# Kernel tuning notes

Hardware: AMD Instinct MI355X
Metric: run time of the kernel (lower is better)

Reference implementation:

```python
import jax, jax.numpy as jnp
import numpy as np
from jax import lax

H = 128

def _lstm_gates(x, h, c, w_ih, w_hh, b_ih, b_hh):
    # PyTorch gate order: i, f, g, o
    g = x @ w_ih.T + h @ w_hh.T + b_ih + b_hh
    i, f, gg, o = jnp.split(g, 4, axis=-1)
    c_new = jax.nn.sigmoid(f) * c + jax.nn.sigmoid(i) * jnp.tanh(gg)
    h_new = jax.nn.sigmoid(o) * jnp.tanh(c_new)
    return h_new, c_new

def _lstm_layer(x_btF, w_ih, w_hh, b_ih, b_hh):
    B = x_btF.shape[0]
    h0 = jnp.zeros((B, H), x_btF.dtype)
    c0 = jnp.zeros((B, H), x_btF.dtype)
    def step(carry, xt):
        h, c = carry
        h, c = _lstm_gates(xt, h, c, w_ih, w_hh, b_ih, b_hh)
        return (h, c), h
    (h_T, c_T), ys = lax.scan(step, (h0, c0), jnp.swapaxes(x_btF, 0, 1))
    return jnp.swapaxes(ys, 0, 1), h_T, c_T

def setup_inputs() -> dict:
    key = jax.random.key(0)
    ks = jax.random.split(key, 20)
    B, T, D, P = 4096, 200, 2, 3
    s = 1.0 / np.sqrt(H)
    u = lambda k, shp: jax.random.uniform(k, shp, jnp.float32, -s, s)
    return {
        'x_hist': jax.random.normal(ks[0], (B, T, D), jnp.float32),
        'params': jax.random.normal(ks[1], (B, P), jnp.float32),
        'pred_len': 200,
        'w_ih0': u(ks[2], (4 * H, D)), 'w_hh0': u(ks[3], (4 * H, H)),
        'b_ih0': u(ks[4], (4 * H,)), 'b_hh0': u(ks[5], (4 * H,)),
        'w_ih1': u(ks[6], (4 * H, H)), 'w_hh1': u(ks[7], (4 * H, H)),
        'b_ih1': u(ks[8], (4 * H,)), 'b_hh1': u(ks[9], (4 * H,)),
        'dec_w_ih': u(ks[10], (4 * H, D + P)), 'dec_w_hh': u(ks[11], (4 * H, H)),
        'dec_b_ih': u(ks[12], (4 * H,)), 'dec_b_hh': u(ks[13], (4 * H,)),
        'proj_w': u(ks[14], (H, P)), 'proj_b': u(ks[15], (H,)),
        'out_w': u(ks[16], (2, H)), 'out_b': u(ks[17], (2,)),
    }

def reference(x_hist, params, pred_len, w_ih0, w_hh0, b_ih0, b_hh0,
              w_ih1, w_hh1, b_ih1, b_hh1, dec_w_ih, dec_w_hh, dec_b_ih,
              dec_b_hh, proj_w, proj_b, out_w, out_b):
    # 2-layer encoder LSTM; only last layer's final (h, c) are used
    y1, _, _ = _lstm_layer(x_hist, w_ih0, w_hh0, b_ih0, b_hh0)
    _, h_n, c_n = _lstm_layer(y1, w_ih1, w_hh1, b_ih1, b_hh1)
    h = h_n + params @ proj_w.T + proj_b
    c = c_n
    cur = x_hist[:, -1, :]
    def step(carry, _):
        h, c, cur = carry
        inp = jnp.concatenate([cur, params], axis=-1)
        h, c = _lstm_gates(inp, h, c, dec_w_ih, dec_w_hh, dec_b_ih, dec_b_hh)
        cur = h @ out_w.T + out_b
        return (h, c, cur), cur
    _, preds = lax.scan(step, (h, c, cur), None, length=pred_len)
    return jnp.swapaxes(preds, 0, 1)  # [B, pred_len, 2]
```

## Files before the change

kernel.cpp:

```cpp
#include <hip/hip_runtime.h>
#include <stdint.h>

typedef __bf16 bf16x8 __attribute__((ext_vector_type(8)));
typedef float  f32x4  __attribute__((ext_vector_type(4)));

#define PRED   200
#define TSTEPS 200
#define NBLK   256

#define ASTR   280
#define ALO    136
#define ABUFE  (16*ASTR*2)
#define W_BYTES 131072
#define A_OFF   W_BYTES
#define LDS_A   (A_OFF + 2*ABUFE)
#define STG_OFF (A_OFF + 2*ABUFE)
#define LDS_C   (STG_OFF + ABUFE)

#define ABUFD  8192
#define LDS_D  (2*ABUFD)

#define STATE_FLOATS ((size_t)NBLK*4*2048)

__device__ __forceinline__ float sigm(float x){ return 1.0f/(1.0f+__expf(-x)); }
__device__ __forceinline__ float tanhx(float x){
  float t=__expf(-2.0f*fabsf(x)); float y=(1.0f-t)/(1.0f+t); return copysignf(y,x);
}
__device__ __forceinline__ bf16x8 hi8(float4 a, float4 b){
  bf16x8 r; r[0]=(__bf16)a.x; r[1]=(__bf16)a.y; r[2]=(__bf16)a.z; r[3]=(__bf16)a.w;
  r[4]=(__bf16)b.x; r[5]=(__bf16)b.y; r[6]=(__bf16)b.z; r[7]=(__bf16)b.w; return r;
}
__device__ __forceinline__ bf16x8 lo8(float4 a, float4 b, bf16x8 h){
  bf16x8 r;
  r[0]=(__bf16)(a.x-(float)h[0]); r[1]=(__bf16)(a.y-(float)h[1]);
  r[2]=(__bf16)(a.z-(float)h[2]); r[3]=(__bf16)(a.w-(float)h[3]);
  r[4]=(__bf16)(b.x-(float)h[4]); r[5]=(__bf16)(b.y-(float)h[5]);
  r[6]=(__bf16)(b.z-(float)h[6]); r[7]=(__bf16)(b.w-(float)h[7]); return r;
}
#define MFMA(A,B,C) __builtin_amdgcn_mfma_f32_16x16x32_bf16((A),(B),(C),0,0,0)

#define PIN(x) do{ \
  unsigned _w0=((unsigned*)&(x))[0], _w1=((unsigned*)&(x))[1], \
           _w2=((unsigned*)&(x))[2], _w3=((unsigned*)&(x))[3]; \
  asm volatile("" : "+v"(_w0), "+v"(_w1), "+v"(_w2), "+v"(_w3)); \
  ((unsigned*)&(x))[0]=_w0; ((unsigned*)&(x))[1]=_w1; \
  ((unsigned*)&(x))[2]=_w2; ((unsigned*)&(x))[3]=_w3; }while(0)
#define PINF(x) asm volatile("" : "+v"(x))

__device__ __forceinline__ void bar_lds(){
  asm volatile("s_waitcnt lgkmcnt(0)" ::: "memory");
  __builtin_amdgcn_s_barrier();
  asm volatile("" ::: "memory");
}

__device__ __forceinline__ int aoff(int row, int col){
  return row*512 + ((((col>>3) ^ (row&7)) << 4) | ((col&7)<<1));
}
__device__ __forceinline__ int frdoff(int c, int qd, int kt, int plane){
  return c*512 + (((((kt<<2)+qd) ^ (c&7)) | (plane<<4)) << 4);
}

__global__ void __launch_bounds__(512,2)
k_l0(const float* __restrict__ xh, const float* __restrict__ wih0,
     const float* __restrict__ whh0, const float* __restrict__ bih0,
     const float* __restrict__ bhh0, float* __restrict__ wsf,
     int chunkStart, int chunkLen, unsigned long long stageFloats)
{
  extern __shared__ char smem[];
  const int tid=threadIdx.x, wv=tid>>6, l=tid&63, c=l&15, qd=l>>4;
  const int hc=wv*16+c, blk=blockIdx.x, r0=blk*16;
  float* stf = wsf + stageFloats;
  #pragma unroll
  for (int i=0;i<16;++i){
    int f=i*8+wv, ntg=f>>2, kt=f&3;
    int g=(ntg&3)*128+(ntg>>2)*16+c, k=kt*32+qd*8;
    const float* s=whh0+g*128+k;
    *(bf16x8*)(smem+f*1024+l*16)=hi8(*(const float4*)s,*(const float4*)(s+4));
  }
  bf16x8 wlo[16];
  #pragma unroll
  for (int tt=0;tt<4;++tt)
    #pragma unroll
    for (int kt=0;kt<4;++kt){
      const float* s=whh0+(size_t)(tt*128+hc)*128+kt*32+qd*8;
      float4 a=*(const float4*)s, b=*(const float4*)(s+4);
      wlo[tt*4+kt]=lo8(a,b,hi8(a,b));
    }
  #pragma unroll
  for (int i=0;i<16;++i) PIN(wlo[i]);
  float b0[4], w0x[4], w0y[4];
  #pragma unroll
  for (int tt=0;tt<4;++tt){
    int g=tt*128+hc;
    b0[tt]=bih0[g]+bhh0[g]; w0x[tt]=wih0[2*g]; w0y[tt]=wih0[2*g+1];
  }
  float c0[4];
  {
    __bf16* B1=(__bf16*)(smem+A_OFF+ABUFE);
    const float* hst=stf+(size_t)(blk*4+0)*2048;
    const float* cst=stf+(size_t)(blk*4+1)*2048;
    #pragma unroll
    for (int i=0;i<4;++i){
      int e=tid*4+i, row=e>>7, col=e&127;
      float v=0.f; if(chunkStart) v=hst[e];
      __bf16 h=(__bf16)v;
      B1[row*ASTR+col]=h; B1[row*ASTR+ALO+col]=(__bf16)(v-(float)h);
    }
    #pragma unroll
    for (int j=0;j<4;++j){ float v=0.f; if(chunkStart) v=cst[(qd*4+j)*128+hc]; c0[j]=v; }
  }
  __syncthreads();
  float hprev[4];
  float2 xv[4];
  #pragma unroll
  for (int j=0;j<4;++j) xv[j]=*(const float2*)(xh+(size_t)(r0+qd*4+j)*400+chunkStart*2);
  for (int t=0;t<chunkLen;++t){
    const int p=t&1, tg=chunkStart+t;
    if (t){
      float* h0p=wsf+((size_t)(t-1)*NBLK+blk)*2048;
      #pragma unroll
      for (int j=0;j<4;++j) h0p[(qd*4+j)*128+hc]=hprev[j];
    }
    float2 xn[4];
    #pragma unroll
    for (int j=0;j<4;++j) xn[j]=(float2){0.f,0.f};
    if (t+1<chunkLen){
      #pragma unroll
      for (int j=0;j<4;++j) xn[j]=*(const float2*)(xh+(size_t)(r0+qd*4+j)*400+(tg+1)*2);
    }
    f32x4 acc[4];
    #pragma unroll
    for (int tt=0;tt<4;++tt) acc[tt]=(f32x4){b0[tt],b0[tt],b0[tt],b0[tt]};
    const char* Ar=smem+A_OFF+(size_t)(1-p)*ABUFE;
    #pragma unroll
    for (int kt=0;kt<4;++kt){
      bf16x8 ah=*(const bf16x8*)(Ar+(c*ASTR+kt*32+qd*8)*2);
      bf16x8 al=*(const bf16x8*)(Ar+(c*ASTR+ALO+kt*32+qd*8)*2);
      #pragma unroll
      for (int tt=0;tt<4;++tt){
        bf16x8 bh=*(const bf16x8*)(smem+(size_t)((wv*4+tt)*4+kt)*1024+l*16);
        acc[tt]=MFMA(ah,bh,acc[tt]);
        acc[tt]=MFMA(al,bh,acc[tt]);
        acc[tt]=MFMA(ah,wlo[tt*4+kt],acc[tt]);
      }
    }
    __bf16* Aw=(__bf16*)(smem+A_OFF+(size_t)p*ABUFE);
    #pragma unroll
    for (int j=0;j<4;++j){
      float gi=acc[0][j]+xv[j].x*w0x[0]+xv[j].y*w0y[0];
      float gf=acc[1][j]+xv[j].x*w0x[1]+xv[j].y*w0y[1];
      float gg=acc[2][j]+xv[j].x*w0x[2]+xv[j].y*w0y[2];
      float go=acc[3][j]+xv[j].x*w0x[3]+xv[j].y*w0y[3];
      float cn=sigm(gf)*c0[j]+sigm(gi)*tanhx(gg); c0[j]=cn;
      float hn=sigm(go)*tanhx(cn);
      int row=qd*4+j;
      __bf16 hh=(__bf16)hn;
      Aw[row*ASTR+hc]=hh; Aw[row*ASTR+ALO+hc]=(__bf16)(hn-(float)hh);
      hprev[j]=hn;
    }
    #pragma unroll
    for (int j=0;j<4;++j) xv[j]=xn[j];
    bar_lds();
  }
  {
    float* h0p=wsf+((size_t)(chunkLen-1)*NBLK+blk)*2048;
    #pragma unroll
    for (int j=0;j<4;++j){
      int row=qd*4+j;
      h0p[row*128+hc]=hprev[j];
      stf[(size_t)(blk*4+0)*2048+row*128+hc]=hprev[j];
      stf[(size_t)(blk*4+1)*2048+row*128+hc]=c0[j];
    }
  }
}

__global__ void __launch_bounds__(512,2)
k_l1(const float* __restrict__ wih1, const float* __restrict__ whh1,
     const float* __restrict__ bih1, const float* __restrict__ bhh1,
     float* __restrict__ wsf, int chunkStart, int chunkLen,
     unsigned long long stageFloats)
{
  extern __shared__ char smem[];
  const int tid=threadIdx.x, wv=tid>>6, l=tid&63, c=l&15, qd=l>>4;
  const int hc=wv*16+c, blk=blockIdx.x;
  float* stf = wsf + stageFloats;
  #pragma unroll
  for (int i=0;i<16;++i){
    int f=i*8+wv, ntg=f>>2, kt=f&3;
    int g=(ntg&3)*128+(ntg>>2)*16+c, k=kt*32+qd*8;
    const float* s=wih1+g*128+k;
    *(bf16x8*)(smem+f*1024+l*16)=hi8(*(const float4*)s,*(const float4*)(s+4));
  }
  bf16x8 whh[16], whl[16], wil[16];
  #pragma unroll
  for (int tt=0;tt<4;++tt)
    #pragma unroll
    for (int kt=0;kt<4;++kt){
      const float* s2=whh1+(size_t)(tt*128+hc)*128+kt*32+qd*8;
      float4 a2=*(const float4*)s2, b2=*(const float4*)(s2+4);
      bf16x8 h2=hi8(a2,b2);
      whh[tt*4+kt]=h2; whl[tt*4+kt]=lo8(a2,b2,h2);
      const float* s3=wih1+(size_t)(tt*128+hc)*128+kt*32+qd*8;
      float4 a3=*(const float4*)s3, b3=*(const float4*)(s3+4);
      wil[tt*4+kt]=lo8(a3,b3,hi8(a3,b3));
    }
  #pragma unroll
  for (int i=0;i<16;++i){ PIN(whh[i]); PIN(whl[i]); PIN(wil[i]); }
  float b1v[4];
  #pragma unroll
  for (int tt=0;tt<4;++tt){ int g=tt*128+hc; b1v[tt]=bih1[g]+bhh1[g]; }
  float c1[4];
  {
    __bf16* B1=(__bf16*)(smem+A_OFF+ABUFE);
    const float* hst=stf+(size_t)(blk*4+2)*2048;
    const float* cst=stf+(size_t)(blk*4+3)*2048;
    #pragma unroll
    for (int i=0;i<4;++i){
      int e=tid*4+i, row=e>>7, col=e&127;
      float v=0.f; if(chunkStart) v=hst[e];
      __bf16 h=(__bf16)v;
      B1[row*ASTR+col]=h; B1[row*ASTR+ALO+col]=(__bf16)(v-(float)h);
    }
    #pragma unroll
    for (int j=0;j<4;++j){ float v=0.f; if(chunkStart) v=cst[(qd*4+j)*128+hc]; c1[j]=v; }
  }
  float4 r4=*(const float4*)(wsf+((size_t)0*NBLK+blk)*2048+tid*4);
  __syncthreads();
  for (int t=0;t<chunkLen;++t){
    const int p=t&1;
    {
      __bf16* ST=(__bf16*)(smem+STG_OFF);
      int e=tid*4, row=e>>7, col=e&127;
      #pragma unroll
      for (int i=0;i<4;++i){
        float v=((const float*)&r4)[i]; __bf16 h=(__bf16)v;
        ST[row*ASTR+col+i]=h; ST[row*ASTR+ALO+col+i]=(__bf16)(v-(float)h);
      }
    }
    if (t+1<chunkLen) r4=*(const float4*)(wsf+((size_t)(t+1)*NBLK+blk)*2048+tid*4);
    bar_lds();
    f32x4 acc[4];
    #pragma unroll
    for (int tt=0;tt<4;++tt) acc[tt]=(f32x4){b1v[tt],b1v[tt],b1v[tt],b1v[tt]};
    const char* Ar=smem+A_OFF+(size_t)(1-p)*ABUFE;
    const char* Sr=smem+STG_OFF;
    #pragma unroll
    for (int kt=0;kt<4;++kt){
      bf16x8 a0h=*(const bf16x8*)(Sr+(c*ASTR+kt*32+qd*8)*2);
      bf16x8 a0l=*(const bf16x8*)(Sr+(c*ASTR+ALO+kt*32+qd*8)*2);
      bf16x8 a1h=*(const bf16x8*)(Ar+(c*ASTR+kt*32+qd*8)*2);
      bf16x8 a1l=*(const bf16x8*)(Ar+(c*ASTR+ALO+kt*32+qd*8)*2);
      #pragma unroll
      for (int tt=0;tt<4;++tt){
        bf16x8 bh=*(const bf16x8*)(smem+(size_t)((wv*4+tt)*4+kt)*1024+l*16);
        acc[tt]=MFMA(a0h,bh,acc[tt]);
        acc[tt]=MFMA(a0l,bh,acc[tt]);
        acc[tt]=MFMA(a0h,wil[tt*4+kt],acc[tt]);
        acc[tt]=MFMA(a1h,whh[tt*4+kt],acc[tt]);
        acc[tt]=MFMA(a1l,whh[tt*4+kt],acc[tt]);
        acc[tt]=MFMA(a1h,whl[tt*4+kt],acc[tt]);
      }
    }
    __bf16* Aw=(__bf16*)(smem+A_OFF+(size_t)p*ABUFE);
    #pragma unroll
    for (int j=0;j<4;++j){
      float cn=sigm(acc[1][j])*c1[j]+sigm(acc[0][j])*tanhx(acc[2][j]); c1[j]=cn;
      float hn=sigm(acc[3][j])*tanhx(cn);
      int row=qd*4+j;
      __bf16 hh=(__bf16)hn;
      Aw[row*ASTR+hc]=hh; Aw[row*ASTR+ALO+hc]=(__bf16)(hn-(float)hh);
      if (t==chunkLen-1){
        stf[(size_t)(blk*4+2)*2048+row*128+hc]=hn;
        stf[(size_t)(blk*4+3)*2048+row*128+hc]=cn;
      }
    }
    bar_lds();
  }
}

__global__ void __launch_bounds__(512,1)
k_dec(const float* __restrict__ xh, const float* __restrict__ pprm,
      const float* __restrict__ dwihp, const float* __restrict__ dwhh,
      const float* __restrict__ dbih, const float* __restrict__ dbhh,
      const float* __restrict__ pw, const float* __restrict__ pb,
      const float* __restrict__ ow, const float* __restrict__ ob,
      const float* __restrict__ wsf, float* __restrict__ out,
      unsigned long long stageFloats)
{
  extern __shared__ char smem[];
  const int tid=threadIdx.x, wv=tid>>6, l=tid&63, c=l&15, qd=l>>4;
  const int hc=wv*16+c, blk=blockIdx.x, r0=blk*16;
  const float* stf = wsf + stageFloats;
  float ob0=ob[0], ob1=ob[1];
  float prm[4][3];
  #pragma unroll
  for (int j=0;j<4;++j){
    size_t r=(size_t)(r0+qd*4+j);
    prm[j][0]=pprm[r*3+0]; prm[j][1]=pprm[r*3+1]; prm[j][2]=pprm[r*3+2];
  }
  float ptF[4][4], dw0[4], dw1[4];
  #pragma unroll
  for (int tt=0;tt<4;++tt){
    int g=tt*128+hc;
    float db=dbih[g]+dbhh[g];
    dw0[tt]=dwihp[g*5+0]; dw1[tt]=dwihp[g*5+1];
    #pragma unroll
    for (int j=0;j<4;++j)
      ptF[tt][j]=db+prm[j][0]*dwihp[g*5+2]+prm[j][1]*dwihp[g*5+3]+prm[j][2]*dwihp[g*5+4]
                 +dw0[tt]*ob0+dw1[tt]*ob1;
  }
  #pragma unroll
  for (int tt=0;tt<4;++tt)
    #pragma unroll
    for (int j=0;j<4;++j) PINF(ptF[tt][j]);
  bf16x8 whi[16], wlo[16];
  #pragma unroll
  for (int tt=0;tt<4;++tt)
    #pragma unroll
    for (int kt=0;kt<4;++kt){
      int g=tt*128+hc, k=kt*32+qd*8;
      float4 a=*(const float4*)(dwhh+(size_t)g*128+k), b=*(const float4*)(dwhh+(size_t)g*128+k+4);
      float4 o0a=*(const float4*)(ow+k),     o0b=*(const float4*)(ow+k+4);
      float4 o1a=*(const float4*)(ow+128+k), o1b=*(const float4*)(ow+128+k+4);
      a.x+=dw0[tt]*o0a.x+dw1[tt]*o1a.x; a.y+=dw0[tt]*o0a.y+dw1[tt]*o1a.y;
      a.z+=dw0[tt]*o0a.z+dw1[tt]*o1a.z; a.w+=dw0[tt]*o0a.w+dw1[tt]*o1a.w;
      b.x+=dw0[tt]*o0b.x+dw1[tt]*o1b.x; b.y+=dw0[tt]*o0b.y+dw1[tt]*o1b.y;
      b.z+=dw0[tt]*o0b.z+dw1[tt]*o1b.z; b.w+=dw0[tt]*o0b.w+dw1[tt]*o1b.w;
      whi[tt*4+kt]=hi8(a,b); wlo[tt*4+kt]=lo8(a,b,whi[tt*4+kt]);
    }
  bf16x8 owh[4], owl[4];
  #pragma unroll
  for (int kt=0;kt<4;++kt){
    int cc=(c<2)?c:0;
    const float* s=ow+cc*128+kt*32+qd*8;
    float4 a=*(const float4*)s, b=*(const float4*)(s+4);
    if (c>=2){ a=(float4){0,0,0,0}; b=(float4){0,0,0,0}; }
    owh[kt]=hi8(a,b); owl[kt]=lo8(a,b,owh[kt]);
  }
  #pragma unroll
  for (int i=0;i<16;++i){ PIN(whi[i]); PIN(wlo[i]); }
  #pragma unroll
  for (int i=0;i<4;++i){ PIN(owh[i]); PIN(owl[i]); }
  const float* h1s=stf+(size_t)(blk*4+2)*2048;
  const float* c1s=stf+(size_t)(blk*4+3)*2048;
  float c1[4], cx0[4], cx1[4];
  {
    float prj0=pw[hc*3+0], prj1=pw[hc*3+1], prj2=pw[hc*3+2], prjb=pb[hc];
    char* B0=smem;
    #pragma unroll
    for (int j=0;j<4;++j){
      int row=qd*4+j;
      float hd=h1s[row*128+hc]+prm[j][0]*prj0+prm[j][1]*prj1+prm[j][2]*prj2+prjb;
      __bf16 h=(__bf16)hd;
      *(__bf16*)(B0+aoff(row,hc))=h;
      *(__bf16*)(B0+aoff(row,hc+128))=(__bf16)(hd-(float)h);
      c1[j]=c1s[row*128+hc];
      float2 xx=*(const float2*)(xh+(size_t)(r0+row)*400+398);
      cx0[j]=xx.x; cx1[j]=xx.y;
    }
  }
  __syncthreads();
  float corr0[4], corr1[4];
  {
    const char* Ar=smem;
    f32x4 pv={0.f,0.f,0.f,0.f};
    #pragma unroll
    for (int kt=0;kt<4;++kt){
      bf16x8 ah=*(const bf16x8*)(Ar+frdoff(c,qd,kt,0));
      bf16x8 al=*(const bf16x8*)(Ar+frdoff(c,qd,kt,1));
      pv=MFMA(ah,owh[kt],pv); pv=MFMA(al,owh[kt],pv); pv=MFMA(ah,owl[kt],pv);
    }
    #pragma unroll
    for (int j=0;j<4;++j){
      float p0=__shfl(pv[j], (l&48),   64);
      float p1=__shfl(pv[j], (l&48)|1, 64);
      corr0[j]=cx0[j]-(p0+ob0);
      corr1[j]=cx1[j]-(p1+ob1);
    }
  }
  f32x4 pvPrev={0.f,0.f,0.f,0.f};
  for (int s=0;s<PRED;++s){
    const int q=s&1;
    if (s>=2 && wv==0 && c<2){
      float obv=c?ob1:ob0;
      #pragma unroll
      for (int j=0;j<4;++j)
        out[(size_t)(r0+qd*4+j)*400+(s-2)*2+c]=pvPrev[j]+obv;
    }
    const char* Ar=smem+(size_t)q*ABUFD;
    f32x4 aA[4];
    #pragma unroll
    for (int tt=0;tt<4;++tt) aA[tt]=(f32x4){ptF[tt][0],ptF[tt][1],ptF[tt][2],ptF[tt][3]};
    #pragma unroll
    for (int kt=0;kt<4;++kt){
      bf16x8 ah=*(const bf16x8*)(Ar+frdoff(c,qd,kt,0));
      bf16x8 al=*(const bf16x8*)(Ar+frdoff(c,qd,kt,1));
      #pragma unroll
      for (int tt=0;tt<4;++tt){
        aA[tt]=MFMA(ah,whi[tt*4+kt],aA[tt]);
        aA[tt]=MFMA(al,whi[tt*4+kt],aA[tt]);
        aA[tt]=MFMA(ah,wlo[tt*4+kt],aA[tt]);
      }
    }
    f32x4 pv={0.f,0.f,0.f,0.f};
    if (wv==0){
      #pragma unroll
      for (int kt=0;kt<4;++kt){
        bf16x8 ah=*(const bf16x8*)(Ar+frdoff(c,qd,kt,0));
        bf16x8 al=*(const bf16x8*)(Ar+frdoff(c,qd,kt,1));
        pv=MFMA(ah,owh[kt],pv); pv=MFMA(al,owh[kt],pv); pv=MFMA(ah,owl[kt],pv);
      }
    }
    char* Aw=smem+(size_t)(1-q)*ABUFD;
    #pragma unroll
    for (int j=0;j<4;++j){
      float gi=aA[0][j];
      float gf=aA[1][j];
      float gg=aA[2][j];
      float go=aA[3][j];
      if (s==0){
        gi+=corr0[j]*dw0[0]+corr1[j]*dw1[0];
        gf+=corr0[j]*dw0[1]+corr1[j]*dw1[1];
        gg+=corr0[j]*dw0[2]+corr1[j]*dw1[2];
        go+=corr0[j]*dw0[3]+corr1[j]*dw1[3];
      }
      float cn=sigm(gf)*c1[j]+sigm(gi)*tanhx(gg); c1[j]=cn;
      float hn=sigm(go)*tanhx(cn);
      int row=qd*4+j;
      __bf16 hh=(__bf16)hn;
      *(__bf16*)(Aw+aoff(row,hc))=hh;
      *(__bf16*)(Aw+aoff(row,hc+128))=(__bf16)(hn-(float)hh);
    }
    if (wv==0) pvPrev=pv;
    bar_lds();
  }
  if (wv==0 && c<2){
    float obv=c?ob1:ob0;
    #pragma unroll
    for (int j=0;j<4;++j)
      out[(size_t)(r0+qd*4+j)*400+(PRED-2)*2+c]=pvPrev[j]+obv;
  }
  if (wv==0){
    const char* Ar=smem+(size_t)(PRED&1)*ABUFD;
    f32x4 pv={0.f,0.f,0.f,0.f};
    #pragma unroll
    for (int kt=0;kt<4;++kt){
      bf16x8 ah=*(const bf16x8*)(Ar+frdoff(c,qd,kt,0));
      bf16x8 al=*(const bf16x8*)(Ar+frdoff(c,qd,kt,1));
      pv=MFMA(ah,owh[kt],pv); pv=MFMA(al,owh[kt],pv); pv=MFMA(ah,owl[kt],pv);
    }
    if (c<2){
      float obv=c?ob1:ob0;
      #pragma unroll
      for (int j=0;j<4;++j)
        out[(size_t)(r0+qd*4+j)*400+(PRED-1)*2+c]=pv[j]+obv;
    }
  }
}

extern "C" void kernel_launch(void* const* d_in, const int* in_sizes, int n_in,
                              void* d_out, int out_size, void* d_ws, size_t ws_size,
                              hipStream_t stream)
{
  (void)out_size;
  const int base = (n_in >= 19 && in_sizes[2] == 1) ? 3 : 2;
  const float* xh   = (const float*)d_in[0];
  const float* prm  = (const float*)d_in[1];
  const float* wih0 = (const float*)d_in[base+0];
  const float* whh0 = (const float*)d_in[base+1];
  const float* bih0 = (const float*)d_in[base+2];
  const float* bhh0 = (const float*)d_in[base+3];
  const float* wih1 = (const float*)d_in[base+4];
  const float* whh1 = (const float*)d_in[base+5];
  const float* bih1 = (const float*)d_in[base+6];
  const float* bhh1 = (const float*)d_in[base+7];
  const float* dwih = (const float*)d_in[base+8];
  const float* dwhh = (const float*)d_in[base+9];
  const float* dbih = (const float*)d_in[base+10];
  const float* dbhh = (const float*)d_in[base+11];
  const float* pw   = (const float*)d_in[base+12];
  const float* pb   = (const float*)d_in[base+13];
  const float* ow   = (const float*)d_in[base+14];
  const float* ob   = (const float*)d_in[base+15];
  float* wsf = (float*)d_ws;

  size_t wsFloats = ws_size / 4;
  size_t avail = (wsFloats > STATE_FLOATS) ? (wsFloats - STATE_FLOATS) : 0;
  int chunkLen = (int)(avail / ((size_t)NBLK * 2048));
  if (chunkLen > 50) chunkLen = 50;
  if (chunkLen < 1)  chunkLen = 1;
  unsigned long long stageFloats = (unsigned long long)chunkLen * NBLK * 2048;

  hipFuncSetAttribute((const void*)k_l0, hipFuncAttributeMaxDynamicSharedMemorySize, LDS_A);
  hipFuncSetAttribute((const void*)k_l1, hipFuncAttributeMaxDynamicSharedMemorySize, LDS_C);

  for (int k0 = 0; k0 < TSTEPS; k0 += chunkLen){
    int len = chunkLen; if (k0 + len > TSTEPS) len = TSTEPS - k0;
    k_l0<<<NBLK,512,LDS_A,stream>>>(xh, wih0, whh0, bih0, bhh0, wsf, k0, len, stageFloats);
    k_l1<<<NBLK,512,LDS_C,stream>>>(wih1, whh1, bih1, bhh1, wsf, k0, len, stageFloats);
  }
  k_dec<<<NBLK,512,LDS_D,stream>>>(xh, prm, dwih, dwhh, dbih, dbhh,
                                   pw, pb, ow, ob, wsf, (float*)d_out, stageFloats);
}
```

Before: 1.845 ms.

## Keep layer-0 recurrent weights in registers and pin two waves per EU

Layer 0 now holds both the high and low bf16 halves of W_hh in VGPRs and no longer stages the high half in LDS. This removes the per-step LDS weight reads and shrinks the kernel's shared-memory footprint to just the activation double buffers. All three kernels get amdgpu_waves_per_eu(2,2), and the decoder's launch bound moves from one block per CU to two. The aim is more resident blocks and fewer LDS reads, at the cost of heavier register pressure that could cause spills.

```diff
diff --git a/kernel.cpp b/kernel.cpp
--- a/kernel.cpp
+++ b/kernel.cpp
@@ -11,9 +11,9 @@
 #define ASTR   280
 #define ALO    136
 #define ABUFE  (16*ASTR*2)
+#define LDS_A  (2*ABUFE)
 #define W_BYTES 131072
 #define A_OFF   W_BYTES
-#define LDS_A   (A_OFF + 2*ABUFE)
 #define STG_OFF (A_OFF + 2*ABUFE)
 #define LDS_C   (STG_OFF + ABUFE)
 
@@ -60,7 +60,7 @@
   return c*512 + (((((kt<<2)+qd) ^ (c&7)) | (plane<<4)) << 4);
 }
 
-__global__ void __launch_bounds__(512,2)
+__global__ void __launch_bounds__(512,2) __attribute__((amdgpu_waves_per_eu(2,2)))
 k_l0(const float* __restrict__ xh, const float* __restrict__ wih0,
      const float* __restrict__ whh0, const float* __restrict__ bih0,
      const float* __restrict__ bhh0, float* __restrict__ wsf,
@@ -70,24 +70,18 @@
   const int tid=threadIdx.x, wv=tid>>6, l=tid&63, c=l&15, qd=l>>4;
   const int hc=wv*16+c, blk=blockIdx.x, r0=blk*16;
   float* stf = wsf + stageFloats;
-  #pragma unroll
-  for (int i=0;i<16;++i){
-    int f=i*8+wv, ntg=f>>2, kt=f&3;
-    int g=(ntg&3)*128+(ntg>>2)*16+c, k=kt*32+qd*8;
-    const float* s=whh0+g*128+k;
-    *(bf16x8*)(smem+f*1024+l*16)=hi8(*(const float4*)s,*(const float4*)(s+4));
-  }
-  bf16x8 wlo[16];
+  bf16x8 whi[16], wlo[16];
   #pragma unroll
   for (int tt=0;tt<4;++tt)
     #pragma unroll
     for (int kt=0;kt<4;++kt){
       const float* s=whh0+(size_t)(tt*128+hc)*128+kt*32+qd*8;
       float4 a=*(const float4*)s, b=*(const float4*)(s+4);
-      wlo[tt*4+kt]=lo8(a,b,hi8(a,b));
-    }
-  #pragma unroll
-  for (int i=0;i<16;++i) PIN(wlo[i]);
+      bf16x8 h=hi8(a,b);
+      whi[tt*4+kt]=h; wlo[tt*4+kt]=lo8(a,b,h);
+    }
+  #pragma unroll
+  for (int i=0;i<16;++i){ PIN(whi[i]); PIN(wlo[i]); }
   float b0[4], w0x[4], w0y[4];
   #pragma unroll
   for (int tt=0;tt<4;++tt){
@@ -96,7 +90,7 @@
   }
   float c0[4];
   {
-    __bf16* B1=(__bf16*)(smem+A_OFF+ABUFE);
+    __bf16* B1=(__bf16*)(smem+ABUFE);
     const float* hst=stf+(size_t)(blk*4+0)*2048;
     const float* cst=stf+(size_t)(blk*4+1)*2048;
     #pragma unroll
@@ -131,20 +125,19 @@
     f32x4 acc[4];
     #pragma unroll
     for (int tt=0;tt<4;++tt) acc[tt]=(f32x4){b0[tt],b0[tt],b0[tt],b0[tt]};
-    const char* Ar=smem+A_OFF+(size_t)(1-p)*ABUFE;
+    const char* Ar=smem+(size_t)(1-p)*ABUFE;
     #pragma unroll
     for (int kt=0;kt<4;++kt){
       bf16x8 ah=*(const bf16x8*)(Ar+(c*ASTR+kt*32+qd*8)*2);
       bf16x8 al=*(const bf16x8*)(Ar+(c*ASTR+ALO+kt*32+qd*8)*2);
       #pragma unroll
       for (int tt=0;tt<4;++tt){
-        bf16x8 bh=*(const bf16x8*)(smem+(size_t)((wv*4+tt)*4+kt)*1024+l*16);
-        acc[tt]=MFMA(ah,bh,acc[tt]);
-        acc[tt]=MFMA(al,bh,acc[tt]);
+        acc[tt]=MFMA(ah,whi[tt*4+kt],acc[tt]);
+        acc[tt]=MFMA(al,whi[tt*4+kt],acc[tt]);
         acc[tt]=MFMA(ah,wlo[tt*4+kt],acc[tt]);
       }
     }
-    __bf16* Aw=(__bf16*)(smem+A_OFF+(size_t)p*ABUFE);
+    __bf16* Aw=(__bf16*)(smem+(size_t)p*ABUFE);
     #pragma unroll
     for (int j=0;j<4;++j){
       float gi=acc[0][j]+xv[j].x*w0x[0]+xv[j].y*w0y[0];
@@ -174,7 +167,7 @@
   }
 }
 
-__global__ void __launch_bounds__(512,2)
+__global__ void __launch_bounds__(512,2) __attribute__((amdgpu_waves_per_eu(2,2)))
 k_l1(const float* __restrict__ wih1, const float* __restrict__ whh1,
      const float* __restrict__ bih1, const float* __restrict__ bhh1,
      float* __restrict__ wsf, int chunkStart, int chunkLen,
@@ -278,7 +271,7 @@
   }
 }
 
-__global__ void __launch_bounds__(512,1)
+__global__ void __launch_bounds__(512,2) __attribute__((amdgpu_waves_per_eu(2,2)))
 k_dec(const float* __restrict__ xh, const float* __restrict__ pprm,
       const float* __restrict__ dwihp, const float* __restrict__ dwhh,
       const float* __restrict__ dbih, const float* __restrict__ dbhh,
```

After: 1.787 ms. -3.2%, faster.
